# Kernel tuning notes

Hardware: AMD Instinct MI355X
Metric: run time of the kernel (lower is better)

The kernel has to match this reference:

```python
import jax, jax.numpy as jnp
import numpy as np

N = 50000       # nodes
E = 800000      # edges
H = 128         # hidden_channels
L = 5           # num_layers
EIN = 16        # edge_in_channels
G = 512         # graphs in batch
NODE_VOCAB = 100
BN_EPS = 1e-5


def setup_inputs() -> dict:
    key = jax.random.key(0)
    ks = jax.random.split(key, 12)
    s = 0.1  # init scale
    return {
        "x": jax.random.randint(ks[0], (N,), 0, NODE_VOCAB, dtype=jnp.int32),
        "edge_index": jax.random.randint(ks[1], (2, E), 0, N, dtype=jnp.int32),
        "edge_attr": jax.random.normal(ks[2], (E, EIN), jnp.float32),
        "batch": jnp.sort(jax.random.randint(ks[3], (N,), 0, G, dtype=jnp.int32)),
        "node_emb": jax.random.normal(ks[4], (NODE_VOCAB, H), jnp.float32) * s,
        "edge_W": jax.random.normal(ks[5], (L, EIN, H), jnp.float32) * s,
        "edge_b": jnp.zeros((L, H), jnp.float32),
        "eps": jnp.zeros((L,), jnp.float32),
        "W1": jax.random.normal(ks[6], (L, H, 2 * H), jnp.float32) * s,
        "b1": jnp.zeros((L, 2 * H), jnp.float32),
        "g1": jnp.ones((L, 2 * H), jnp.float32),
        "be1": jnp.zeros((L, 2 * H), jnp.float32),
        "W2": jax.random.normal(ks[7], (L, 2 * H, H), jnp.float32) * s,
        "b2": jnp.zeros((L, H), jnp.float32),
        "bn_g": jnp.ones((L, H), jnp.float32),
        "bn_b": jnp.zeros((L, H), jnp.float32),
        "out_W": jax.random.normal(ks[8], (H, H), jnp.float32) * s,
        "out_b": jnp.zeros((H,), jnp.float32),
    }


def _bn(h, gamma, beta):
    # training-mode BatchNorm1d: batch statistics over the node axis
    m = h.mean(0)
    v = jnp.mean((h - m) ** 2, axis=0)
    return (h - m) * jax.lax.rsqrt(v + BN_EPS) * gamma + beta


def reference(x, edge_index, edge_attr, batch, node_emb, edge_W, edge_b, eps,
              W1, b1, g1, be1, W2, b2, bn_g, bn_b, out_W, out_b):
    h = node_emb[x]                                   # [N,H] node encoder
    src, dst = edge_index[0], edge_index[1]
    for i in range(L):
        # EGINConv: edge encode, gather->relu->scatter-add, GIN MLP
        e = edge_attr @ edge_W[i] + edge_b[i]         # [E,H]
        msg = jax.nn.relu(h[src] + e)                 # gather + relu
        agg = jax.ops.segment_sum(msg, dst, num_segments=N)  # scatter-add
        z = (1.0 + eps[i]) * h + agg
        z = jax.nn.relu(_bn(z @ W1[i] + b1[i], g1[i], be1[i]))  # mlp inner
        h = _bn(z @ W2[i] + b2[i], bn_g[i], bn_b[i])  # inter-layer BN
        if i < L - 1:
            h = jax.nn.relu(h)                        # dropout: eval (identity)
    # global_mean_pool
    sums = jax.ops.segment_sum(h, batch, num_segments=G)
    cnt = jax.ops.segment_sum(jnp.ones((N, 1), h.dtype), batch, num_segments=G)
    pooled = sums / jnp.maximum(cnt, 1.0)
    return pooled @ out_W + out_b                     # [G,H]
```

## Files before the change

kernel.cpp:

```cpp
#include <hip/hip_runtime.h>
#include <hip/hip_fp16.h>

#define N_NODES 50000
#define N_EDGES 800000
#define HD 128
#define NLAYERS 5
#define EINC 16
#define NG 512

typedef _Float16 half8 __attribute__((ext_vector_type(8)));
typedef float f32x4 __attribute__((ext_vector_type(4)));
typedef float f32x2 __attribute__((ext_vector_type(2)));

__global__ __launch_bounds__(256) void k_embed(const int* __restrict__ x,
                                               const float* __restrict__ emb,
                                               float* __restrict__ h) {
  int i = blockIdx.x * 256 + threadIdx.x;
  if (i < N_NODES * 32) {
    int n = i >> 5, cv = i & 31;
    *(float4*)&h[n * HD + cv * 4] = *(const float4*)&emb[x[n] * HD + cv * 4];
  }
}

__global__ __launch_bounds__(256) void k_hist(const int* __restrict__ ei,
                                              int* __restrict__ deg) {
  int e = blockIdx.x * 256 + threadIdx.x;
  if (e < N_EDGES) atomicAdd(&deg[ei[N_EDGES + e]], 1);
}

__global__ __launch_bounds__(256) void k_scan1(const int* __restrict__ deg,
                                               int* __restrict__ incl,
                                               int* __restrict__ bsum) {
  __shared__ int s[256];
  int i = blockIdx.x * 256 + threadIdx.x;
  int v = (i < N_NODES) ? deg[i] : 0;
  s[threadIdx.x] = v;
  __syncthreads();
  for (int d = 1; d < 256; d <<= 1) {
    int t = (threadIdx.x >= d) ? s[threadIdx.x - d] : 0;
    __syncthreads();
    s[threadIdx.x] += t;
    __syncthreads();
  }
  if (i < N_NODES) incl[i] = s[threadIdx.x];
  if (threadIdx.x == 255) bsum[blockIdx.x] = s[255];
}

__global__ void k_scan2(int* __restrict__ bsum, int nb) {
  __shared__ int s[256];
  int v = (threadIdx.x < nb) ? bsum[threadIdx.x] : 0;
  s[threadIdx.x] = v;
  __syncthreads();
  for (int d = 1; d < 256; d <<= 1) {
    int t = (threadIdx.x >= d) ? s[threadIdx.x - d] : 0;
    __syncthreads();
    s[threadIdx.x] += t;
    __syncthreads();
  }
  if (threadIdx.x < nb) bsum[threadIdx.x] = s[threadIdx.x];
}

__global__ __launch_bounds__(256) void k_scan3(const int* __restrict__ deg,
                                               const int* __restrict__ incl,
                                               const int* __restrict__ bsum,
                                               int* __restrict__ offs,
                                               int* __restrict__ cursor) {
  int i = blockIdx.x * 256 + threadIdx.x;
  if (i < N_NODES) {
    int base = (blockIdx.x > 0) ? bsum[blockIdx.x - 1] : 0;
    int start = base + incl[i] - deg[i];
    offs[i] = start;
    cursor[i] = start;
    if (i == N_NODES - 1) offs[N_NODES] = N_EDGES;
  }
}

__global__ __launch_bounds__(256) void k_scatter(const int* __restrict__ ei,
                                                 const float* __restrict__ ea,
                                                 int* __restrict__ cursor,
                                                 int* __restrict__ srcs,
                                                 int* __restrict__ eids,
                                                 float* __restrict__ ea_s,
                                                 int permuted) {
  int e = blockIdx.x * 256 + threadIdx.x;
  if (e < N_EDGES) {
    int dst = ei[N_EDGES + e];
    int pos = atomicAdd(&cursor[dst], 1);
    srcs[pos] = ei[e];
    eids[pos] = e;
    if (permuted) {
      float4 a0 = *(const float4*)&ea[(size_t)e * EINC];
      float4 a1 = *(const float4*)&ea[(size_t)e * EINC + 4];
      float4 a2 = *(const float4*)&ea[(size_t)e * EINC + 8];
      float4 a3 = *(const float4*)&ea[(size_t)e * EINC + 12];
      *(float4*)&ea_s[(size_t)pos * EINC] = a0;
      *(float4*)&ea_s[(size_t)pos * EINC + 4] = a1;
      *(float4*)&ea_s[(size_t)pos * EINC + 8] = a2;
      *(float4*)&ea_s[(size_t)pos * EINC + 12] = a3;
    }
  }
}

__global__ __launch_bounds__(256) void k_cvtw1(const float* __restrict__ W1,
                                               _Float16* __restrict__ w1t) {
  int i = blockIdx.x * 256 + threadIdx.x;
  if (i < NLAYERS * 256 * 128) {
    int l = i >> 15, r = i & 32767;
    int n = r >> 7, k = r & 127;
    w1t[i] = (_Float16)W1[(size_t)l * 32768 + k * 256 + n];
  }
}
__global__ __launch_bounds__(256) void k_cvtw2(const float* __restrict__ W2,
                                               _Float16* __restrict__ w2t) {
  int i = blockIdx.x * 256 + threadIdx.x;
  if (i < NLAYERS * 128 * 256) {
    int l = i >> 15, r = i & 32767;
    int n = r >> 8, k = r & 255;
    w2t[i] = (_Float16)W2[(size_t)l * 32768 + k * 128 + n];
  }
}

__global__ __launch_bounds__(256) void k_aggr(const int* __restrict__ offs,
                                              const int* __restrict__ srcs,
                                              const int* __restrict__ eids,
                                              const float* __restrict__ ea,
                                              const float* __restrict__ ea_s,
                                              const float* __restrict__ W,
                                              const float* __restrict__ eb,
                                              const float* __restrict__ epsA, int layer,
                                              const float* __restrict__ h,
                                              float* __restrict__ z,
                                              int permuted) {
  const int wid = threadIdx.x >> 6;
  const int lane = threadIdx.x & 63;
  int n = blockIdx.x * 4 + wid;
  if (n >= N_NODES) return;
  const int c0 = lane * 2;

  f32x2 wp[EINC];
#pragma unroll
  for (int k = 0; k < EINC; ++k) wp[k] = *(const f32x2*)&W[k * HD + c0];
  const f32x2 ebp = *(const f32x2*)&eb[c0];
  const float epsv = 1.0f + epsA[layer];
  const f32x2 zero = {0.f, 0.f};

  int j0 = offs[n], j1 = offs[n + 1];
  f32x2 hn = *(const f32x2*)&h[(size_t)n * HD + c0];
  f32x2 acc;
  acc[0] = epsv * hn[0];
  acc[1] = epsv * hn[1];

  if (permuted) {
    int j = j0;
    for (; j + 3 < j1; j += 4) {
      int js = __builtin_amdgcn_readfirstlane(j);
      const float* ra = &ea_s[(size_t)js * EINC];
      int s0 = srcs[j], s1 = srcs[j + 1], s2 = srcs[j + 2], s3 = srcs[j + 3];
      f32x2 g0 = *(const f32x2*)&h[(size_t)s0 * HD + c0];
      f32x2 g1 = *(const f32x2*)&h[(size_t)s1 * HD + c0];
      f32x2 g2 = *(const f32x2*)&h[(size_t)s2 * HD + c0];
      f32x2 g3 = *(const f32x2*)&h[(size_t)s3 * HD + c0];
      f32x2 e0 = ebp, e1 = ebp, e2 = ebp, e3 = ebp;
#pragma unroll
      for (int k = 0; k < EINC; ++k) {
        f32x2 w2 = wp[k];
        float a0 = ra[k], a1 = ra[EINC + k], a2 = ra[2 * EINC + k], a3 = ra[3 * EINC + k];
        f32x2 v0 = {a0, a0}, v1 = {a1, a1}, v2 = {a2, a2}, v3 = {a3, a3};
        e0 = __builtin_elementwise_fma(v0, w2, e0);
        e1 = __builtin_elementwise_fma(v1, w2, e1);
        e2 = __builtin_elementwise_fma(v2, w2, e2);
        e3 = __builtin_elementwise_fma(v3, w2, e3);
      }
      acc += __builtin_elementwise_max(g0 + e0, zero);
      acc += __builtin_elementwise_max(g1 + e1, zero);
      acc += __builtin_elementwise_max(g2 + e2, zero);
      acc += __builtin_elementwise_max(g3 + e3, zero);
    }
    for (; j < j1; ++j) {
      int js = __builtin_amdgcn_readfirstlane(j);
      const float* ra = &ea_s[(size_t)js * EINC];
      int s0 = srcs[j];
      f32x2 g0 = *(const f32x2*)&h[(size_t)s0 * HD + c0];
      f32x2 e0 = ebp;
#pragma unroll
      for (int k = 0; k < EINC; ++k) {
        float a0 = ra[k];
        f32x2 v0 = {a0, a0};
        e0 = __builtin_elementwise_fma(v0, wp[k], e0);
      }
      acc += __builtin_elementwise_max(g0 + e0, zero);
    }
  } else {
    for (int j = j0; j < j1; ++j) {
      int eid = __builtin_amdgcn_readfirstlane(eids[j]);
      const float* ra = &ea[(size_t)eid * EINC];
      int s0 = srcs[j];
      f32x2 g0 = *(const f32x2*)&h[(size_t)s0 * HD + c0];
      f32x2 e0 = ebp;
#pragma unroll
      for (int k = 0; k < EINC; ++k) {
        float a0 = ra[k];
        f32x2 v0 = {a0, a0};
        e0 = __builtin_elementwise_fma(v0, wp[k], e0);
      }
      acc += __builtin_elementwise_max(g0 + e0, zero);
    }
  }
  *(f32x2*)&z[(size_t)n * HD + c0] = acc;
}

__global__ __launch_bounds__(256) void k_gemm1m(const float* __restrict__ z,
                                                const _Float16* __restrict__ w1t,
                                                const float* __restrict__ bias,
                                                _Float16* __restrict__ y1h,
                                                float* __restrict__ gsum,
                                                float* __restrict__ gsq) {
  __shared__ _Float16 sA[128 * 40];
  __shared__ _Float16 sBT[128 * 40];
  __shared__ float ssum[128], ssq[128];
  const int tid = threadIdx.x;
  const int lane = tid & 63;
  const int wid = tid >> 6;
  const int wm = wid >> 1, wn = wid & 1;
  const int m0 = blockIdx.x * 128;
  const int n0 = blockIdx.y * 128;

  if (tid < 128) { ssum[tid] = 0.f; ssq[tid] = 0.f; }

  f32x4 acc[4][4];
  const f32x4 zz = {0.f, 0.f, 0.f, 0.f};
#pragma unroll
  for (int a = 0; a < 4; ++a)
#pragma unroll
    for (int b = 0; b < 4; ++b) acc[a][b] = zz;

  const int srow = tid >> 1;
  const int skh = (tid & 1) * 16;

  for (int k0 = 0; k0 < 128; k0 += 32) {
    {
      int n = m0 + srow;
      half8 p0, p1;
      if (n < N_NODES) {
        float4 a0 = *(const float4*)&z[(size_t)n * 128 + k0 + skh + 0];
        float4 a1 = *(const float4*)&z[(size_t)n * 128 + k0 + skh + 4];
        float4 a2 = *(const float4*)&z[(size_t)n * 128 + k0 + skh + 8];
        float4 a3 = *(const float4*)&z[(size_t)n * 128 + k0 + skh + 12];
        p0[0] = (_Float16)a0.x; p0[1] = (_Float16)a0.y; p0[2] = (_Float16)a0.z; p0[3] = (_Float16)a0.w;
        p0[4] = (_Float16)a1.x; p0[5] = (_Float16)a1.y; p0[6] = (_Float16)a1.z; p0[7] = (_Float16)a1.w;
        p1[0] = (_Float16)a2.x; p1[1] = (_Float16)a2.y; p1[2] = (_Float16)a2.z; p1[3] = (_Float16)a2.w;
        p1[4] = (_Float16)a3.x; p1[5] = (_Float16)a3.y; p1[6] = (_Float16)a3.z; p1[7] = (_Float16)a3.w;
      } else {
#pragma unroll
        for (int j = 0; j < 8; ++j) { p0[j] = (_Float16)0.f; p1[j] = (_Float16)0.f; }
      }
      *(half8*)&sA[srow * 40 + skh] = p0;
      *(half8*)&sA[srow * 40 + skh + 8] = p1;
    }
    {
      half8 u0 = *(const half8*)&w1t[(size_t)(n0 + srow) * 128 + k0 + skh];
      half8 u1 = *(const half8*)&w1t[(size_t)(n0 + srow) * 128 + k0 + skh + 8];
      *(half8*)&sBT[srow * 40 + skh] = u0;
      *(half8*)&sBT[srow * 40 + skh + 8] = u1;
    }
    __syncthreads();
    half8 af[4], bf[4];
#pragma unroll
    for (int t = 0; t < 4; ++t) {
      af[t] = *(const half8*)&sA[(wm * 64 + t * 16 + (lane & 15)) * 40 + (lane >> 4) * 8];
      bf[t] = *(const half8*)&sBT[(wn * 64 + t * 16 + (lane & 15)) * 40 + (lane >> 4) * 8];
    }
#pragma unroll
    for (int tm = 0; tm < 4; ++tm)
#pragma unroll
      for (int tn = 0; tn < 4; ++tn)
        acc[tm][tn] = __builtin_amdgcn_mfma_f32_16x16x32_f16(af[tm], bf[tn], acc[tm][tn], 0, 0, 0);
    __syncthreads();
  }

  float bsv[4];
#pragma unroll
  for (int tn = 0; tn < 4; ++tn) bsv[tn] = bias[n0 + wn * 64 + tn * 16 + (lane & 15)];
  float sacc[4] = {0.f, 0.f, 0.f, 0.f}, qacc[4] = {0.f, 0.f, 0.f, 0.f};
#pragma unroll
  for (int tm = 0; tm < 4; ++tm) {
    int nbase = m0 + wm * 64 + tm * 16 + (lane >> 4) * 4;
#pragma unroll
    for (int r = 0; r < 4; ++r) {
      int n = nbase + r;
      if (n < N_NODES) {
#pragma unroll
        for (int tn = 0; tn < 4; ++tn) {
          float v = acc[tm][tn][r] + bsv[tn];
          y1h[(size_t)n * 256 + n0 + wn * 64 + tn * 16 + (lane & 15)] = (_Float16)v;
          sacc[tn] += v; qacc[tn] += v * v;
        }
      }
    }
  }
#pragma unroll
  for (int tn = 0; tn < 4; ++tn) {
    int c = wn * 64 + tn * 16 + (lane & 15);
    atomicAdd(&ssum[c], sacc[tn]);
    atomicAdd(&ssq[c], qacc[tn]);
  }
  __syncthreads();
  if (tid < 128) {
    unsafeAtomicAdd(&gsum[n0 + tid], ssum[tid]);
    unsafeAtomicAdd(&gsq[n0 + tid], ssq[tid]);
  }
}

__global__ __launch_bounds__(256) void k_gemm2m(const _Float16* __restrict__ y1h,
                                                const float* __restrict__ sc,
                                                const float* __restrict__ sh,
                                                const _Float16* __restrict__ w2t,
                                                const float* __restrict__ bias,
                                                float* __restrict__ y2,
                                                float* __restrict__ gsum,
                                                float* __restrict__ gsq) {
  __shared__ _Float16 sA[64 * 40];
  __shared__ _Float16 sBT[128 * 40];
  __shared__ float ssc[256], ssh[256];
  __shared__ float ssum[128], ssq[128];
  const int tid = threadIdx.x;
  const int lane = tid & 63;
  const int wid = tid >> 6;
  const int wm = wid >> 1, wn = wid & 1;
  const int m0 = blockIdx.x * 64;

  ssc[tid] = sc[tid];
  ssh[tid] = sh[tid];
  if (tid < 128) { ssum[tid] = 0.f; ssq[tid] = 0.f; }
  __syncthreads();

  f32x4 acc[2][4];
  const f32x4 zz = {0.f, 0.f, 0.f, 0.f};
#pragma unroll
  for (int a = 0; a < 2; ++a)
#pragma unroll
    for (int b = 0; b < 4; ++b) acc[a][b] = zz;

  const int arow = tid >> 2;
  const int akq = (tid & 3) * 8;
  const int brow = tid >> 1;
  const int bkh = (tid & 1) * 16;

  for (int k0 = 0; k0 < 256; k0 += 32) {
    {
      int n = m0 + arow;
      half8 p;
      if (n < N_NODES) {
        half8 yv = *(const half8*)&y1h[(size_t)n * 256 + k0 + akq];
#pragma unroll
        for (int j = 0; j < 8; ++j) {
          float v = fmaxf((float)yv[j] * ssc[k0 + akq + j] + ssh[k0 + akq + j], 0.f);
          p[j] = (_Float16)v;
        }
      } else {
#pragma unroll
        for (int j = 0; j < 8; ++j) p[j] = (_Float16)0.f;
      }
      *(half8*)&sA[arow * 40 + akq] = p;
    }
    {
      half8 u0 = *(const half8*)&w2t[(size_t)brow * 256 + k0 + bkh];
      half8 u1 = *(const half8*)&w2t[(size_t)brow * 256 + k0 + bkh + 8];
      *(half8*)&sBT[brow * 40 + bkh] = u0;
      *(half8*)&sBT[brow * 40 + bkh + 8] = u1;
    }
    __syncthreads();
    half8 af[2], bf[4];
#pragma unroll
    for (int t = 0; t < 2; ++t)
      af[t] = *(const half8*)&sA[(wm * 32 + t * 16 + (lane & 15)) * 40 + (lane >> 4) * 8];
#pragma unroll
    for (int t = 0; t < 4; ++t)
      bf[t] = *(const half8*)&sBT[(wn * 64 + t * 16 + (lane & 15)) * 40 + (lane >> 4) * 8];
#pragma unroll
    for (int tm = 0; tm < 2; ++tm)
#pragma unroll
      for (int tn = 0; tn < 4; ++tn)
        acc[tm][tn] = __builtin_amdgcn_mfma_f32_16x16x32_f16(af[tm], bf[tn], acc[tm][tn], 0, 0, 0);
    __syncthreads();
  }

  float bsv[4];
#pragma unroll
  for (int tn = 0; tn < 4; ++tn) bsv[tn] = bias[wn * 64 + tn * 16 + (lane & 15)];
  float sacc[4] = {0.f, 0.f, 0.f, 0.f}, qacc[4] = {0.f, 0.f, 0.f, 0.f};
#pragma unroll
  for (int tm = 0; tm < 2; ++tm) {
    int nbase = m0 + wm * 32 + tm * 16 + (lane >> 4) * 4;
#pragma unroll
    for (int r = 0; r < 4; ++r) {
      int n = nbase + r;
      if (n < N_NODES) {
#pragma unroll
        for (int tn = 0; tn < 4; ++tn) {
          float v = acc[tm][tn][r] + bsv[tn];
          y2[(size_t)n * 128 + wn * 64 + tn * 16 + (lane & 15)] = v;
          sacc[tn] += v; qacc[tn] += v * v;
        }
      }
    }
  }
#pragma unroll
  for (int tn = 0; tn < 4; ++tn) {
    int c = wn * 64 + tn * 16 + (lane & 15);
    atomicAdd(&ssum[c], sacc[tn]);
    atomicAdd(&ssq[c], qacc[tn]);
  }
  __syncthreads();
  if (tid < 128) {
    unsafeAtomicAdd(&gsum[tid], ssum[tid]);
    unsafeAtomicAdd(&gsq[tid], ssq[tid]);
  }
}

__global__ void k_bnfin(const float* __restrict__ sum, const float* __restrict__ sq,
                        const float* __restrict__ g, const float* __restrict__ b,
                        float* __restrict__ sc, float* __restrict__ sh, int C) {
  int c = blockIdx.x * blockDim.x + threadIdx.x;
  if (c < C) {
    const float invN = 1.0f / (float)N_NODES;
    float m = sum[c] * invN;
    float v = fmaxf(sq[c] * invN - m * m, 0.0f);
    float rs = rsqrtf(v + 1e-5f);
    float scale = g[c] * rs;
    sc[c] = scale;
    sh[c] = b[c] - m * scale;
  }
}

__global__ __launch_bounds__(256) void k_bnapply(const float* __restrict__ y2,
                                                 const float* __restrict__ sc,
                                                 const float* __restrict__ sh,
                                                 float* __restrict__ h, int dorelu) {
  int i = blockIdx.x * 256 + threadIdx.x;
  if (i < N_NODES * 32) {
    int cv = i & 31;
    float4 v = *(const float4*)&y2[i * 4];
    float4 s4 = *(const float4*)&sc[cv * 4];
    float4 h4 = *(const float4*)&sh[cv * 4];
    float4 o;
    o.x = v.x * s4.x + h4.x; o.y = v.y * s4.y + h4.y;
    o.z = v.z * s4.z + h4.z; o.w = v.w * s4.w + h4.w;
    if (dorelu) {
      o.x = fmaxf(o.x, 0.f); o.y = fmaxf(o.y, 0.f);
      o.z = fmaxf(o.z, 0.f); o.w = fmaxf(o.w, 0.f);
    }
    *(float4*)&h[i * 4] = o;
  }
}

__global__ void k_goff(const int* __restrict__ batch, int* __restrict__ goff) {
  int g = blockIdx.x * blockDim.x + threadIdx.x;
  if (g <= NG) {
    if (g == NG) { goff[g] = N_NODES; return; }
    int lo = 0, hi = N_NODES;
    while (lo < hi) { int mid = (lo + hi) >> 1; if (batch[mid] < g) lo = mid + 1; else hi = mid; }
    goff[g] = lo;
  }
}

__global__ __launch_bounds__(256) void k_poolseg(const float* __restrict__ h,
                                                 const int* __restrict__ goff,
                                                 float* __restrict__ pooled) {
  __shared__ float sred[256];
  int g = blockIdx.x;
  int c = threadIdx.x & 127;
  int half = threadIdx.x >> 7;
  int n0 = goff[g], n1 = goff[g + 1];
  float s = 0.f;
  for (int n = n0 + half; n < n1; n += 2) s += h[(size_t)n * HD + c];
  sred[threadIdx.x] = s;
  __syncthreads();
  if (threadIdx.x < 128) {
    float tot = sred[threadIdx.x] + sred[threadIdx.x + 128];
    float cntf = (float)(n1 - n0);
    pooled[g * HD + threadIdx.x] = tot / fmaxf(cntf, 1.0f);
  }
}

__global__ __launch_bounds__(128) void k_final(const float* __restrict__ pooled,
                                               const float* __restrict__ oW,
                                               const float* __restrict__ ob,
                                               float* __restrict__ out) {
  __shared__ float sP[HD];
  int g = blockIdx.x;
  int c = threadIdx.x;
  sP[c] = pooled[g * HD + c];
  __syncthreads();
  float acc = ob[c];
#pragma unroll 8
  for (int k = 0; k < HD; ++k) acc += sP[k] * oW[k * HD + c];
  out[g * HD + c] = acc;
}

extern "C" void kernel_launch(void* const* d_in, const int* in_sizes, int n_in,
                              void* d_out, int out_size, void* d_ws, size_t ws_size,
                              hipStream_t stream) {
  const int* x = (const int*)d_in[0];
  const int* ei = (const int*)d_in[1];
  const float* ea = (const float*)d_in[2];
  const int* batch = (const int*)d_in[3];
  const float* emb = (const float*)d_in[4];
  const float* eW = (const float*)d_in[5];
  const float* eb = (const float*)d_in[6];
  const float* epsA = (const float*)d_in[7];
  const float* W1 = (const float*)d_in[8];
  const float* b1 = (const float*)d_in[9];
  const float* g1 = (const float*)d_in[10];
  const float* be1 = (const float*)d_in[11];
  const float* W2 = (const float*)d_in[12];
  const float* b2 = (const float*)d_in[13];
  const float* bng = (const float*)d_in[14];
  const float* bnb = (const float*)d_in[15];
  const float* oW = (const float*)d_in[16];
  const float* ob = (const float*)d_in[17];
  float* out = (float*)d_out;

  int* ip = (int*)d_ws;
  int* deg = ip;
  int* incl = deg + 50000;
  int* offs = incl + 50000;
  int* cursor = offs + 50001;
  int* srcs = cursor + 50000;
  int* eids = srcs + 800000;
  int* bsum = eids + 800000;
  int* goff = bsum + 200;
  float* fp = (float*)(ip + 1800916);
  float* h = fp;
  float* zbuf = h + 6400000;
  _Float16* y1h = (_Float16*)(zbuf + 6400000);
  float* stats = zbuf + 12800000;
  float* sc1 = stats + 768;
  float* sh1 = sc1 + 256;
  float* sc2 = sh1 + 256;
  float* sh2 = sc2 + 128;
  float* pooled = sh2 + 128;
  _Float16* w1t = (_Float16*)(pooled + 65536);
  _Float16* w2t = w1t + 163840;
  float* ea_s = pooled + 65536 + 163840;

  size_t needed_with = (size_t)(ea_s + 12800000 - (float*)d_ws) * 4;
  int permuted = (ws_size >= needed_with) ? 1 : 0;

  const int vec_blocks = (N_NODES * 32 + 255) / 256;
  const int edge_blocks = (N_EDGES + 255) / 256;
  const int node_blocks = (N_NODES + 255) / 256;

  k_embed<<<vec_blocks, 256, 0, stream>>>(x, emb, h);

  hipMemsetAsync(deg, 0, 50000 * sizeof(int), stream);
  k_hist<<<edge_blocks, 256, 0, stream>>>(ei, deg);
  k_scan1<<<node_blocks, 256, 0, stream>>>(deg, incl, bsum);
  k_scan2<<<1, 256, 0, stream>>>(bsum, node_blocks);
  k_scan3<<<node_blocks, 256, 0, stream>>>(deg, incl, bsum, offs, cursor);
  k_scatter<<<edge_blocks, 256, 0, stream>>>(ei, ea, cursor, srcs, eids, ea_s, permuted);
  k_goff<<<3, 256, 0, stream>>>(batch, goff);
  k_cvtw1<<<640, 256, 0, stream>>>(W1, w1t);
  k_cvtw2<<<640, 256, 0, stream>>>(W2, w2t);

  for (int l = 0; l < NLAYERS; ++l) {
    hipMemsetAsync(stats, 0, 768 * sizeof(float), stream);
    k_aggr<<<(N_NODES + 3) / 4, 256, 0, stream>>>(offs, srcs, eids, ea, ea_s,
                                                  eW + (size_t)l * EINC * HD, eb + l * HD,
                                                  epsA, l, h, zbuf, permuted);
    k_gemm1m<<<dim3(391, 2), 256, 0, stream>>>(zbuf, w1t + (size_t)l * 32768,
                                               b1 + l * 256, y1h, stats, stats + 256);
    k_bnfin<<<1, 256, 0, stream>>>(stats, stats + 256, g1 + l * 256, be1 + l * 256, sc1, sh1, 256);
    k_gemm2m<<<782, 256, 0, stream>>>(y1h, sc1, sh1, w2t + (size_t)l * 32768,
                                      b2 + l * HD, zbuf, stats + 512, stats + 640);
    k_bnfin<<<1, 128, 0, stream>>>(stats + 512, stats + 640, bng + l * HD, bnb + l * HD, sc2, sh2, 128);
    k_bnapply<<<vec_blocks, 256, 0, stream>>>(zbuf, sc2, sh2, h, (l < NLAYERS - 1) ? 1 : 0);
  }

  k_poolseg<<<NG, 256, 0, stream>>>(h, goff, pooled);
  k_final<<<NG, 128, 0, stream>>>(pooled, oW, ob, out);
}
```

Before: 1.094 ms.

## Fuse batchnorm apply into aggregation gather and final pooling

Removes the per-layer BN-apply pass by having gemm2 write raw pre-BN output into h and applying scale/shift+ReLU on the fly when gathering neighbor rows in the aggregation kernel. The last layer's BN is folded into the pooling since the mean pool is linear. This saves a full read/write pass over the node features per layer at the cost of extra FMAs on every gathered edge row. It also skips writing edge ids when the permuted layout is used.

```diff
diff --git a/kernel.cpp b/kernel.cpp
--- a/kernel.cpp
+++ b/kernel.cpp
@@ -87,7 +87,6 @@
     int dst = ei[N_EDGES + e];
     int pos = atomicAdd(&cursor[dst], 1);
     srcs[pos] = ei[e];
-    eids[pos] = e;
     if (permuted) {
       float4 a0 = *(const float4*)&ea[(size_t)e * EINC];
       float4 a1 = *(const float4*)&ea[(size_t)e * EINC + 4];
@@ -97,6 +96,8 @@
       *(float4*)&ea_s[(size_t)pos * EINC + 4] = a1;
       *(float4*)&ea_s[(size_t)pos * EINC + 8] = a2;
       *(float4*)&ea_s[(size_t)pos * EINC + 12] = a3;
+    } else {
+      eids[pos] = e;
     }
   }
 }
@@ -128,7 +129,10 @@
                                               const float* __restrict__ W,
                                               const float* __restrict__ eb,
                                               const float* __restrict__ epsA, int layer,
-                                              const float* __restrict__ h,
+                                              const float* __restrict__ hraw,
+                                              const float* __restrict__ bnsc,
+                                              const float* __restrict__ bnsh,
+                                              int fuse_bn,
                                               float* __restrict__ z,
                                               int permuted) {
   const int wid = threadIdx.x >> 6;
@@ -143,9 +147,15 @@
   const f32x2 ebp = *(const f32x2*)&eb[c0];
   const float epsv = 1.0f + epsA[layer];
   const f32x2 zero = {0.f, 0.f};
+  f32x2 scp = {1.f, 1.f}, shp = {0.f, 0.f};
+  if (fuse_bn) {
+    scp = *(const f32x2*)&bnsc[c0];
+    shp = *(const f32x2*)&bnsh[c0];
+  }
 
   int j0 = offs[n], j1 = offs[n + 1];
-  f32x2 hn = *(const f32x2*)&h[(size_t)n * HD + c0];
+  f32x2 hn = *(const f32x2*)&hraw[(size_t)n * HD + c0];
+  if (fuse_bn) hn = __builtin_elementwise_max(__builtin_elementwise_fma(hn, scp, shp), zero);
   f32x2 acc;
   acc[0] = epsv * hn[0];
   acc[1] = epsv * hn[1];
@@ -156,10 +166,16 @@
       int js = __builtin_amdgcn_readfirstlane(j);
       const float* ra = &ea_s[(size_t)js * EINC];
       int s0 = srcs[j], s1 = srcs[j + 1], s2 = srcs[j + 2], s3 = srcs[j + 3];
-      f32x2 g0 = *(const f32x2*)&h[(size_t)s0 * HD + c0];
-      f32x2 g1 = *(const f32x2*)&h[(size_t)s1 * HD + c0];
-      f32x2 g2 = *(const f32x2*)&h[(size_t)s2 * HD + c0];
-      f32x2 g3 = *(const f32x2*)&h[(size_t)s3 * HD + c0];
+      f32x2 g0 = *(const f32x2*)&hraw[(size_t)s0 * HD + c0];
+      f32x2 g1 = *(const f32x2*)&hraw[(size_t)s1 * HD + c0];
+      f32x2 g2 = *(const f32x2*)&hraw[(size_t)s2 * HD + c0];
+      f32x2 g3 = *(const f32x2*)&hraw[(size_t)s3 * HD + c0];
+      if (fuse_bn) {
+        g0 = __builtin_elementwise_max(__builtin_elementwise_fma(g0, scp, shp), zero);
+        g1 = __builtin_elementwise_max(__builtin_elementwise_fma(g1, scp, shp), zero);
+        g2 = __builtin_elementwise_max(__builtin_elementwise_fma(g2, scp, shp), zero);
+        g3 = __builtin_elementwise_max(__builtin_elementwise_fma(g3, scp, shp), zero);
+      }
       f32x2 e0 = ebp, e1 = ebp, e2 = ebp, e3 = ebp;
 #pragma unroll
       for (int k = 0; k < EINC; ++k) {
@@ -180,7 +196,8 @@
       int js = __builtin_amdgcn_readfirstlane(j);
       const float* ra = &ea_s[(size_t)js * EINC];
       int s0 = srcs[j];
-      f32x2 g0 = *(const f32x2*)&h[(size_t)s0 * HD + c0];
+      f32x2 g0 = *(const f32x2*)&hraw[(size_t)s0 * HD + c0];
+      if (fuse_bn) g0 = __builtin_elementwise_max(__builtin_elementwise_fma(g0, scp, shp), zero);
       f32x2 e0 = ebp;
 #pragma unroll
       for (int k = 0; k < EINC; ++k) {
@@ -195,7 +212,8 @@
       int eid = __builtin_amdgcn_readfirstlane(eids[j]);
       const float* ra = &ea[(size_t)eid * EINC];
       int s0 = srcs[j];
-      f32x2 g0 = *(const f32x2*)&h[(size_t)s0 * HD + c0];
+      f32x2 g0 = *(const f32x2*)&hraw[(size_t)s0 * HD + c0];
+      if (fuse_bn) g0 = __builtin_elementwise_max(__builtin_elementwise_fma(g0, scp, shp), zero);
       f32x2 e0 = ebp;
 #pragma unroll
       for (int k = 0; k < EINC; ++k) {
@@ -433,27 +451,6 @@
   }
 }
 
-__global__ __launch_bounds__(256) void k_bnapply(const float* __restrict__ y2,
-                                                 const float* __restrict__ sc,
-                                                 const float* __restrict__ sh,
-                                                 float* __restrict__ h, int dorelu) {
-  int i = blockIdx.x * 256 + threadIdx.x;
-  if (i < N_NODES * 32) {
-    int cv = i & 31;
-    float4 v = *(const float4*)&y2[i * 4];
-    float4 s4 = *(const float4*)&sc[cv * 4];
-    float4 h4 = *(const float4*)&sh[cv * 4];
-    float4 o;
-    o.x = v.x * s4.x + h4.x; o.y = v.y * s4.y + h4.y;
-    o.z = v.z * s4.z + h4.z; o.w = v.w * s4.w + h4.w;
-    if (dorelu) {
-      o.x = fmaxf(o.x, 0.f); o.y = fmaxf(o.y, 0.f);
-      o.z = fmaxf(o.z, 0.f); o.w = fmaxf(o.w, 0.f);
-    }
-    *(float4*)&h[i * 4] = o;
-  }
-}
-
 __global__ void k_goff(const int* __restrict__ batch, int* __restrict__ goff) {
   int g = blockIdx.x * blockDim.x + threadIdx.x;
   if (g <= NG) {
@@ -464,7 +461,9 @@
   }
 }
 
-__global__ __launch_bounds__(256) void k_poolseg(const float* __restrict__ h,
+__global__ __launch_bounds__(256) void k_poolseg(const float* __restrict__ y2raw,
+                                                 const float* __restrict__ sc,
+                                                 const float* __restrict__ sh,
                                                  const int* __restrict__ goff,
                                                  float* __restrict__ pooled) {
   __shared__ float sred[256];
@@ -473,13 +472,13 @@
   int half = threadIdx.x >> 7;
   int n0 = goff[g], n1 = goff[g + 1];
   float s = 0.f;
-  for (int n = n0 + half; n < n1; n += 2) s += h[(size_t)n * HD + c];
+  for (int n = n0 + half; n < n1; n += 2) s += y2raw[(size_t)n * HD + c];
   sred[threadIdx.x] = s;
   __syncthreads();
   if (threadIdx.x < 128) {
     float tot = sred[threadIdx.x] + sred[threadIdx.x + 128];
-    float cntf = (float)(n1 - n0);
-    pooled[g * HD + threadIdx.x] = tot / fmaxf(cntf, 1.0f);
+    float cntf = fmaxf((float)(n1 - n0), 1.0f);
+    pooled[g * HD + threadIdx.x] = sc[threadIdx.x] * (tot / cntf) + sh[threadIdx.x];
   }
 }
 
@@ -567,16 +566,16 @@
     hipMemsetAsync(stats, 0, 768 * sizeof(float), stream);
     k_aggr<<<(N_NODES + 3) / 4, 256, 0, stream>>>(offs, srcs, eids, ea, ea_s,
                                                   eW + (size_t)l * EINC * HD, eb + l * HD,
-                                                  epsA, l, h, zbuf, permuted);
+                                                  epsA, l, h, sc2, sh2, (l > 0) ? 1 : 0,
+                                                  zbuf, permuted);
     k_gemm1m<<<dim3(391, 2), 256, 0, stream>>>(zbuf, w1t + (size_t)l * 32768,
                                                b1 + l * 256, y1h, stats, stats + 256);
     k_bnfin<<<1, 256, 0, stream>>>(stats, stats + 256, g1 + l * 256, be1 + l * 256, sc1, sh1, 256);
     k_gemm2m<<<782, 256, 0, stream>>>(y1h, sc1, sh1, w2t + (size_t)l * 32768,
-                                      b2 + l * HD, zbuf, stats + 512, stats + 640);
+                                      b2 + l * HD, h, stats + 512, stats + 640);
     k_bnfin<<<1, 128, 0, stream>>>(stats + 512, stats + 640, bng + l * HD, bnb + l * HD, sc2, sh2, 128);
-    k_bnapply<<<vec_blocks, 256, 0, stream>>>(zbuf, sc2, sh2, h, (l < NLAYERS - 1) ? 1 : 0);
-  }
-
-  k_poolseg<<<NG, 256, 0, stream>>>(h, goff, pooled);
+  }
+
+  k_poolseg<<<NG, 256, 0, stream>>>(h, sc2, sh2, goff, pooled);
   k_final<<<NG, 128, 0, stream>>>(pooled, oW, ob, out);
 }
```

After: 1.071 ms. -2.1%, faster.
